# Performance work log

Measured on AMD Instinct MI355X. Metric: run time of the kernel, lower is better.

The kernel has to match this reference:

```python
import jax, jax.numpy as jnp
import numpy as np

B, T, C, H = 128, 256, 512, 512

def setup_inputs() -> dict:
    key = jax.random.key(0)
    k1, k2, k3, k4 = jax.random.split(key, 4)
    x = jax.random.normal(k1, (B, T, C), dtype=jnp.float32)
    # nn.Linear(n_embed, H_size, bias=False).weight has shape [H, C]; scaled init
    s = 1.0 / np.sqrt(C)
    Wq = jax.random.normal(k2, (H, C), dtype=jnp.float32) * s
    Wk = jax.random.normal(k3, (H, C), dtype=jnp.float32) * s
    Wv = jax.random.normal(k4, (H, C), dtype=jnp.float32) * s
    return {"x": x, "Wq": Wq, "Wk": Wk, "Wv": Wv}

def reference(x, Wq, Wk, Wv):
    # q,k,v: [B,T,H] = x @ W.T (torch Linear convention)
    q = jnp.einsum('btc,hc->bth', x, Wq)
    k = jnp.einsum('btc,hc->bth', x, Wk)
    v = jnp.einsum('btc,hc->bth', x, Wv)
    scale = k.shape[-1] ** -0.5
    score = jnp.einsum('bqh,bkh->bqk', q, k) * scale  # [B,T,T]
    # causal mask: position j attends to i only if i <= j
    i = jnp.arange(T)
    causal = i[None, :] <= i[:, None]  # [T,T] lower-triangular
    score = jnp.where(causal[None, :, :], score, -jnp.inf)
    attn = jax.nn.softmax(score, axis=-1)
    # dropout is identity in eval mode
    out = jnp.einsum('bqk,bkh->bqh', attn, v)  # [B,T,H]
    return out
```

## Files before the change

### kernel.cpp

```cpp
#include <hip/hip_runtime.h>

#define B_ 128
#define T_ 256
#define C_ 512
#define H_ 512
#define CSCALE 0.063763824f

typedef _Float16 f16x8 __attribute__((ext_vector_type(8)));
typedef _Float16 f16x4 __attribute__((ext_vector_type(4)));
typedef _Float16 f16x2 __attribute__((ext_vector_type(2)));
typedef float    f32x4 __attribute__((ext_vector_type(4)));
typedef float    f32x16 __attribute__((ext_vector_type(16)));
typedef unsigned int u32;
typedef u32 u32x4 __attribute__((ext_vector_type(4)));

__device__ __forceinline__ void gld16(const void* gsrc, void* ldst) {
  __builtin_amdgcn_global_load_lds(
      (__attribute__((address_space(1))) void*)gsrc,
      (__attribute__((address_space(3))) void*)ldst, 16, 0, 0);
}

__global__ __launch_bounds__(256) void cvt_kernel(
    const float4* __restrict__ x, const float4* __restrict__ wq,
    const float4* __restrict__ wk, const float4* __restrict__ wv,
    f16x4* __restrict__ dst) {
  const int NX = (B_ * T_ * C_) / 4;
  const int NW = (H_ * C_) / 4;
  const int total = NX + 3 * NW;
  int gid = blockIdx.x * 256 + threadIdx.x;
  int gsz = gridDim.x * 256;
  for (int i = gid; i < total; i += gsz) {
    float4 f;
    if (i < NX)            f = x[i];
    else if (i < NX + NW)  f = wq[i - NX];
    else if (i < NX + 2*NW) f = wk[i - NX - NW];
    else                   f = wv[i - NX - 2*NW];
    f16x4 u = {(_Float16)f.x, (_Float16)f.y, (_Float16)f.z, (_Float16)f.w};
    dst[i] = u;
  }
}

__global__ __launch_bounds__(256, 2) void proj_kernel(
    const _Float16* __restrict__ xh, const _Float16* __restrict__ wh,
    _Float16* __restrict__ qh, _Float16* __restrict__ kh,
    _Float16* __restrict__ vth) {
  __shared__ _Float16 L[3][2][4096];

  const int tid  = threadIdx.x;
  const int lane = tid & 63;
  const int wave = tid >> 6;
  const int lr = lane & 15, lk = lane >> 4;
  const int lane8 = lane * 8;
  const int m0 = blockIdx.x * 128;
  const int n0 = blockIdx.y * 128;
  const int z  = blockIdx.z;
  const _Float16* wz = wh + z * (H_ * C_);

  const int wm = (wave >> 1) * 64;
  const int wn = (wave & 1) * 64;
  const int ga = (wave >> 1) * 4;
  const int gb = (wave & 1) * 4;

  const _Float16* aS = xh + (size_t)(m0 + wave * 16 + lr) * C_ + lk * 8;
  const _Float16* bS = wz + (size_t)(n0 + wave * 16 + lr) * C_ + lk * 8;

  f32x4 acc[4][4];
#pragma unroll
  for (int i = 0; i < 4; ++i)
#pragma unroll
    for (int j = 0; j < 4; ++j) acc[i][j] = {0.f, 0.f, 0.f, 0.f};

#define STAGE(RB, K0) do {                                                    \
    gld16((const void*)(aS + (K0)),            (void*)&L[RB][0][wave * 512]); \
    gld16((const void*)(aS + 64 * C_ + (K0)),  (void*)&L[RB][0][(4 + wave) * 512]); \
    gld16((const void*)(bS + (K0)),            (void*)&L[RB][1][wave * 512]); \
    gld16((const void*)(bS + 64 * C_ + (K0)),  (void*)&L[RB][1][(4 + wave) * 512]); \
  } while (0)

  STAGE(0, 0);
  STAGE(1, 32);
  asm volatile("s_waitcnt vmcnt(4)" ::: "memory");
  __builtin_amdgcn_s_barrier();

#pragma unroll 1
  for (int t = 0; t < 16; ++t) {
    const int rb = t % 3;

    f16x8 af[4], bf[4];
#pragma unroll
    for (int mi = 0; mi < 4; ++mi)
      af[mi] = *(const f16x8*)&L[rb][0][(ga + mi) * 512 + lane8];
#pragma unroll
    for (int ni = 0; ni < 4; ++ni)
      bf[ni] = *(const f16x8*)&L[rb][1][(gb + ni) * 512 + lane8];

    if (t + 2 < 16) STAGE((t + 2) % 3, (t + 2) * 32);

    __builtin_amdgcn_s_setprio(1);
#pragma unroll
    for (int mi = 0; mi < 4; ++mi)
#pragma unroll
      for (int ni = 0; ni < 4; ++ni)
        acc[mi][ni] = __builtin_amdgcn_mfma_f32_16x16x32_f16(
            af[mi], bf[ni], acc[mi][ni], 0, 0, 0);
    __builtin_amdgcn_s_setprio(0);

    if (t + 2 < 16)      asm volatile("s_waitcnt vmcnt(4)" ::: "memory");
    else if (t == 14)    asm volatile("s_waitcnt vmcnt(0)" ::: "memory");
    __builtin_amdgcn_s_barrier();
  }
#undef STAGE

  if (z < 2) {
    _Float16* out = (z == 0) ? qh : kh;
#pragma unroll
    for (int mi = 0; mi < 4; ++mi) {
      int mg = m0 + wm + mi * 16 + lk * 4;
#pragma unroll
      for (int ni = 0; ni < 4; ++ni) {
        int n = n0 + wn + ni * 16 + lr;
#pragma unroll
        for (int r = 0; r < 4; ++r)
          out[(size_t)(mg + r) * H_ + n] = (_Float16)acc[mi][ni][r];
      }
    }
  } else {
#pragma unroll
    for (int mi = 0; mi < 4; ++mi) {
      int mbase = m0 + wm + mi * 16 + lk * 4;
      int bb = mbase >> 8, tt = mbase & 255;
#pragma unroll
      for (int ni = 0; ni < 4; ++ni) {
        int n = n0 + wn + ni * 16 + lr;
        f16x4 u = {(_Float16)acc[mi][ni][0], (_Float16)acc[mi][ni][1],
                   (_Float16)acc[mi][ni][2], (_Float16)acc[mi][ni][3]};
        *(f16x4*)&vth[(size_t)bb * (H_ * T_) + (size_t)n * T_ + tt] = u;
      }
    }
  }
}

__global__ __launch_bounds__(256, 2) void attn_kernel(
    const _Float16* __restrict__ qh, const _Float16* __restrict__ kh,
    const _Float16* __restrict__ vth, float* __restrict__ dout) {
  __shared__ f32x4 Ex[2][4][4][64];

  const int tid  = threadIdx.x;
  const int lane = tid & 63;
  const int wq   = tid >> 6;
  const int lq   = lane & 31;
  const int hi   = lane >> 5;
  const int flat = blockIdx.x;
  const int xcd  = flat & 7;
  const int rest = flat >> 3;
  const int qb   = 7 - (rest & 7);
  const int g    = rest >> 3;
  const int b    = xcd + (g << 3);
  const int q0   = qb * 32;
  const int nkv  = qb + 1;
  const int hbase = wq * 128;
  const int qg   = q0 + lq;

  f16x8 qf[8];
  const _Float16* qp = qh + ((size_t)b * T_ + qg) * H_ + hbase + hi * 8;
#pragma unroll
  for (int ks = 0; ks < 8; ++ks) qf[ks] = *(const f16x8*)&qp[ks * 16];

  f32x16 ot[4];
#pragma unroll
  for (int i = 0; i < 4; ++i) ot[i] = {};
  float m_ = -1e30f, l_ = 0.f;

  const _Float16* kp = kh  + ((size_t)b * T_ + lq) * H_ + hbase + hi * 8;
  const _Float16* vp = vth + ((size_t)b * H_ + hbase + lq) * T_ + hi * 8;

  f16x8 kf[8];
#pragma unroll
  for (int ks = 0; ks < 8; ++ks) kf[ks] = *(const f16x8*)&kp[ks * 16];
  {
    f32x16 s2 = {};
#pragma unroll
    for (int ks = 0; ks < 8; ++ks)
      s2 = __builtin_amdgcn_mfma_f32_32x32x16_f16(kf[ks], qf[ks], s2, 0, 0, 0);
#pragma unroll
    for (int c = 0; c < 4; ++c) {
      f32x4 w4 = {s2[c*4+0], s2[c*4+1], s2[c*4+2], s2[c*4+3]};
      Ex[0][wq][c][lane] = w4;
    }
  }

  for (int kvt = 0; kvt < nkv; ++kvt) {
    const int kv0 = kvt * 32;
    const int buf = kvt & 1;
    const bool more = (kvt + 1 < nkv);
    __syncthreads();

    f32x16 st;
#pragma unroll
    for (int c = 0; c < 4; ++c) {
      f32x4 r0 = Ex[buf][0][c][lane];
      f32x4 r1 = Ex[buf][1][c][lane];
      f32x4 r2 = Ex[buf][2][c][lane];
      f32x4 r3 = Ex[buf][3][c][lane];
      f32x4 r = (r0 + r1) + (r2 + r3);
      st[c*4+0] = r[0]; st[c*4+1] = r[1]; st[c*4+2] = r[2]; st[c*4+3] = r[3];
    }

    if (more) {
#pragma unroll
      for (int ks = 0; ks < 8; ++ks)
        kf[ks] = *(const f16x8*)&kp[(size_t)(kv0 + 32) * H_ + ks * 16];
    }

    float rm = -1e30f;
    const int kvb = kv0 + 4 * hi;
#pragma unroll
    for (int r = 0; r < 16; ++r) {
      int kvg = kvb + (r & 3) + 8 * (r >> 2);
      float v = (kvg > qg) ? -1e30f : st[r];
      st[r] = v;
      rm = fmaxf(rm, v);
    }
    rm = fmaxf(rm, __shfl_xor(rm, 32, 64));

    if (__any((int)(rm > m_ + 64.f))) {
      float mn = fmaxf(m_, rm);
      float al = __builtin_amdgcn_exp2f((m_ - mn) * CSCALE);
      m_ = mn; l_ *= al;
#pragma unroll
      for (int i = 0; i < 4; ++i)
#pragma unroll
        for (int e = 0; e < 16; ++e) ot[i][e] *= al;
    }
    float rs = 0.f;
#pragma unroll
    for (int r = 0; r < 16; ++r) {
      st[r] = __builtin_amdgcn_exp2f((st[r] - m_) * CSCALE);
      rs += st[r];
    }
    rs += __shfl_xor(rs, 32, 64);
    l_ += rs;

    f16x8 pb0, pb1;
    {
      f16x2 h0 = {(_Float16)st[0], (_Float16)st[1]};
      f16x2 h1 = {(_Float16)st[2], (_Float16)st[3]};
      f16x2 h2 = {(_Float16)st[4], (_Float16)st[5]};
      f16x2 h3 = {(_Float16)st[6], (_Float16)st[7]};
      u32 w0 = __builtin_bit_cast(u32, h0), w1 = __builtin_bit_cast(u32, h1);
      u32 w2 = __builtin_bit_cast(u32, h2), w3 = __builtin_bit_cast(u32, h3);
      u32 s0 = (u32)__shfl_xor((int)w0, 32, 64);
      u32 s1 = (u32)__shfl_xor((int)w1, 32, 64);
      u32 s2 = (u32)__shfl_xor((int)w2, 32, 64);
      u32 s3 = (u32)__shfl_xor((int)w3, 32, 64);
      u32x4 t0 = { hi ? s2 : w0, hi ? s3 : w1, hi ? w2 : s0, hi ? w3 : s1 };
      pb0 = __builtin_bit_cast(f16x8, t0);
    }
    {
      f16x2 h0 = {(_Float16)st[8],  (_Float16)st[9]};
      f16x2 h1 = {(_Float16)st[10], (_Float16)st[11]};
      f16x2 h2 = {(_Float16)st[12], (_Float16)st[13]};
      f16x2 h3 = {(_Float16)st[14], (_Float16)st[15]};
      u32 w0 = __builtin_bit_cast(u32, h0), w1 = __builtin_bit_cast(u32, h1);
      u32 w2 = __builtin_bit_cast(u32, h2), w3 = __builtin_bit_cast(u32, h3);
      u32 s0 = (u32)__shfl_xor((int)w0, 32, 64);
      u32 s1 = (u32)__shfl_xor((int)w1, 32, 64);
      u32 s2 = (u32)__shfl_xor((int)w2, 32, 64);
      u32 s3 = (u32)__shfl_xor((int)w3, 32, 64);
      u32x4 t1 = { hi ? s2 : w0, hi ? s3 : w1, hi ? w2 : s0, hi ? w3 : s1 };
      pb1 = __builtin_bit_cast(f16x8, t1);
    }

    __builtin_amdgcn_s_setprio(1);
#pragma unroll
    for (int ht = 0; ht < 4; ++ht) {
      f16x8 va0 = *(const f16x8*)&vp[(size_t)(ht * 32) * T_ + kv0];
      f16x8 va1 = *(const f16x8*)&vp[(size_t)(ht * 32) * T_ + kv0 + 16];
      ot[ht] = __builtin_amdgcn_mfma_f32_32x32x16_f16(va0, pb0, ot[ht], 0, 0, 0);
      ot[ht] = __builtin_amdgcn_mfma_f32_32x32x16_f16(va1, pb1, ot[ht], 0, 0, 0);
    }
    __builtin_amdgcn_s_setprio(0);

    if (more) {
      f32x16 s2v = {};
      __builtin_amdgcn_s_setprio(1);
#pragma unroll
      for (int ks = 0; ks < 8; ++ks)
        s2v = __builtin_amdgcn_mfma_f32_32x32x16_f16(kf[ks], qf[ks], s2v, 0, 0, 0);
      __builtin_amdgcn_s_setprio(0);
#pragma unroll
      for (int c = 0; c < 4; ++c) {
        f32x4 w4 = {s2v[c*4+0], s2v[c*4+1], s2v[c*4+2], s2v[c*4+3]};
        Ex[buf ^ 1][wq][c][lane] = w4;
      }
    }
  }

  float li = 1.0f / l_;
  float* op = dout + ((size_t)b * T_ + qg) * H_ + hbase + 4 * hi;
#pragma unroll
  for (int ht = 0; ht < 4; ++ht)
#pragma unroll
    for (int rq = 0; rq < 4; ++rq) {
      f32x4 v4 = {ot[ht][rq*4+0] * li, ot[ht][rq*4+1] * li,
                  ot[ht][rq*4+2] * li, ot[ht][rq*4+3] * li};
      *(f32x4*)&op[ht * 32 + rq * 8] = v4;
    }
}

extern "C" void kernel_launch(void* const* d_in, const int* in_sizes, int n_in,
                              void* d_out, int out_size, void* d_ws, size_t ws_size,
                              hipStream_t stream) {
  const size_t NXE = (size_t)B_ * T_ * C_;
  const size_t NWE = (size_t)3 * H_ * C_;
  const size_t NQE = (size_t)B_ * T_ * H_;
  const size_t need = (NXE + NWE + 3 * NQE) * sizeof(_Float16);
  if (ws_size < need) return;

  const float* x  = (const float*)d_in[0];
  const float* wq = (const float*)d_in[1];
  const float* wk = (const float*)d_in[2];
  const float* wv = (const float*)d_in[3];

  _Float16* xh  = (_Float16*)d_ws;
  _Float16* wh  = xh + NXE;
  _Float16* qh  = wh + NWE;
  _Float16* kh  = qh + NQE;
  _Float16* vth = kh + NQE;

  cvt_kernel<<<2048, 256, 0, stream>>>((const float4*)x, (const float4*)wq,
                                       (const float4*)wk, (const float4*)wv,
                                       (f16x4*)xh);
  proj_kernel<<<dim3(256, 4, 3), dim3(256), 0, stream>>>(xh, wh, qh, kh, vth);
  attn_kernel<<<1024, 256, 0, stream>>>(qh, kh, vth, (float*)d_out);
}
```

Before: 202.0 us.

## Simplify projection GEMM to single-buffer LDS loop and split conversion kernels

The projection kernel drops its triple-buffered global_load_lds pipeline with manual waitcnt and setprio in favour of a simple single-buffered loop bracketed by two __syncthreads per K step. The fp32-to-fp16 conversion is split into separate kernels for x and for the weights. The attention kernel now loads K fragments inline instead of prefetching them into registers, and its launch bound is raised to 3 blocks per SM to cut register use and raise occupancy. The cost is losing load/compute overlap in the GEMM and adding an extra kernel launch.

```diff
diff --git a/kernel.cpp b/kernel.cpp
--- a/kernel.cpp
+++ b/kernel.cpp
@@ -20,37 +20,40 @@
       (__attribute__((address_space(3))) void*)ldst, 16, 0, 0);
 }
 
-__global__ __launch_bounds__(256) void cvt_kernel(
-    const float4* __restrict__ x, const float4* __restrict__ wq,
-    const float4* __restrict__ wk, const float4* __restrict__ wv,
-    f16x4* __restrict__ dst) {
+__global__ __launch_bounds__(256) void cvtx_kernel(
+    const float4* __restrict__ x, f16x4* __restrict__ dst) {
   const int NX = (B_ * T_ * C_) / 4;
-  const int NW = (H_ * C_) / 4;
-  const int total = NX + 3 * NW;
   int gid = blockIdx.x * 256 + threadIdx.x;
   int gsz = gridDim.x * 256;
-  for (int i = gid; i < total; i += gsz) {
-    float4 f;
-    if (i < NX)            f = x[i];
-    else if (i < NX + NW)  f = wq[i - NX];
-    else if (i < NX + 2*NW) f = wk[i - NX - NW];
-    else                   f = wv[i - NX - 2*NW];
+  for (int i = gid; i < NX; i += gsz) {
+    float4 f = x[i];
     f16x4 u = {(_Float16)f.x, (_Float16)f.y, (_Float16)f.z, (_Float16)f.w};
     dst[i] = u;
   }
 }
 
-__global__ __launch_bounds__(256, 2) void proj_kernel(
+__global__ __launch_bounds__(256) void cvtw_kernel(
+    const float4* __restrict__ wq, const float4* __restrict__ wk,
+    const float4* __restrict__ wv, f16x4* __restrict__ dst) {
+  const int NW = (H_ * C_) / 4;
+  int i = blockIdx.x * 256 + threadIdx.x;
+  if (i >= 3 * NW) return;
+  float4 f = (i < NW) ? wq[i] : (i < 2 * NW ? wk[i - NW] : wv[i - 2 * NW]);
+  f16x4 u = {(_Float16)f.x, (_Float16)f.y, (_Float16)f.z, (_Float16)f.w};
+  dst[i] = u;
+}
+
+__global__ __launch_bounds__(256) void proj_kernel(
     const _Float16* __restrict__ xh, const _Float16* __restrict__ wh,
     _Float16* __restrict__ qh, _Float16* __restrict__ kh,
     _Float16* __restrict__ vth) {
-  __shared__ _Float16 L[3][2][4096];
+  __shared__ _Float16 As[128 * 32];
+  __shared__ _Float16 Bs[128 * 32];
 
   const int tid  = threadIdx.x;
   const int lane = tid & 63;
   const int wave = tid >> 6;
   const int lr = lane & 15, lk = lane >> 4;
-  const int lane8 = lane * 8;
   const int m0 = blockIdx.x * 128;
   const int n0 = blockIdx.y * 128;
   const int z  = blockIdx.z;
@@ -58,11 +61,6 @@
 
   const int wm = (wave >> 1) * 64;
   const int wn = (wave & 1) * 64;
-  const int ga = (wave >> 1) * 4;
-  const int gb = (wave & 1) * 4;
-
-  const _Float16* aS = xh + (size_t)(m0 + wave * 16 + lr) * C_ + lk * 8;
-  const _Float16* bS = wz + (size_t)(n0 + wave * 16 + lr) * C_ + lk * 8;
 
   f32x4 acc[4][4];
 #pragma unroll
@@ -70,58 +68,44 @@
 #pragma unroll
     for (int j = 0; j < 4; ++j) acc[i][j] = {0.f, 0.f, 0.f, 0.f};
 
-#define STAGE(RB, K0) do {                                                    \
-    gld16((const void*)(aS + (K0)),            (void*)&L[RB][0][wave * 512]); \
-    gld16((const void*)(aS + 64 * C_ + (K0)),  (void*)&L[RB][0][(4 + wave) * 512]); \
-    gld16((const void*)(bS + (K0)),            (void*)&L[RB][1][wave * 512]); \
-    gld16((const void*)(bS + 64 * C_ + (K0)),  (void*)&L[RB][1][(4 + wave) * 512]); \
-  } while (0)
-
-  STAGE(0, 0);
-  STAGE(1, 32);
-  asm volatile("s_waitcnt vmcnt(4)" ::: "memory");
-  __builtin_amdgcn_s_barrier();
-
-#pragma unroll 1
-  for (int t = 0; t < 16; ++t) {
-    const int rb = t % 3;
-
-    f16x8 af[4], bf[4];
+  const int srow = tid >> 2, scol = (tid & 3) * 8;
+  const _Float16* aSrc = xh + (size_t)(m0 + srow) * C_ + scol;
+  const _Float16* bSrc = wz + (size_t)(n0 + srow) * C_ + scol;
+
+  for (int k0 = 0; k0 < C_; k0 += 32) {
+    __syncthreads();
+#pragma unroll
+    for (int i = 0; i < 2; ++i) {
+      gld16((const void*)(aSrc + i * 64 * C_ + k0), (void*)&As[i * 2048 + wave * 512]);
+      gld16((const void*)(bSrc + i * 64 * C_ + k0), (void*)&Bs[i * 2048 + wave * 512]);
+    }
+    __syncthreads();
+
+    f16x8 a[4], b[4];
 #pragma unroll
     for (int mi = 0; mi < 4; ++mi)
-      af[mi] = *(const f16x8*)&L[rb][0][(ga + mi) * 512 + lane8];
+      a[mi] = *(const f16x8*)&As[(wm + mi * 16 + lr) * 32 + lk * 8];
 #pragma unroll
     for (int ni = 0; ni < 4; ++ni)
-      bf[ni] = *(const f16x8*)&L[rb][1][(gb + ni) * 512 + lane8];
-
-    if (t + 2 < 16) STAGE((t + 2) % 3, (t + 2) * 32);
-
-    __builtin_amdgcn_s_setprio(1);
+      b[ni] = *(const f16x8*)&Bs[(wn + ni * 16 + lr) * 32 + lk * 8];
 #pragma unroll
     for (int mi = 0; mi < 4; ++mi)
 #pragma unroll
       for (int ni = 0; ni < 4; ++ni)
-        acc[mi][ni] = __builtin_amdgcn_mfma_f32_16x16x32_f16(
-            af[mi], bf[ni], acc[mi][ni], 0, 0, 0);
-    __builtin_amdgcn_s_setprio(0);
-
-    if (t + 2 < 16)      asm volatile("s_waitcnt vmcnt(4)" ::: "memory");
-    else if (t == 14)    asm volatile("s_waitcnt vmcnt(0)" ::: "memory");
-    __builtin_amdgcn_s_barrier();
-  }
-#undef STAGE
+        acc[mi][ni] = __builtin_amdgcn_mfma_f32_16x16x32_f16(a[mi], b[ni], acc[mi][ni], 0, 0, 0);
+  }
 
   if (z < 2) {
     _Float16* out = (z == 0) ? qh : kh;
 #pragma unroll
     for (int mi = 0; mi < 4; ++mi) {
-      int mg = m0 + wm + mi * 16 + lk * 4;
+      int mbase = m0 + wm + mi * 16 + lk * 4;
 #pragma unroll
       for (int ni = 0; ni < 4; ++ni) {
         int n = n0 + wn + ni * 16 + lr;
 #pragma unroll
         for (int r = 0; r < 4; ++r)
-          out[(size_t)(mg + r) * H_ + n] = (_Float16)acc[mi][ni][r];
+          out[(size_t)(mbase + r) * H_ + n] = (_Float16)acc[mi][ni][r];
       }
     }
   } else {
@@ -140,7 +124,7 @@
   }
 }
 
-__global__ __launch_bounds__(256, 2) void attn_kernel(
+__global__ __launch_bounds__(256, 3) void attn_kernel(
     const _Float16* __restrict__ qh, const _Float16* __restrict__ kh,
     const _Float16* __restrict__ vth, float* __restrict__ dout) {
   __shared__ f32x4 Ex[2][4][4][64];
@@ -174,14 +158,13 @@
   const _Float16* kp = kh  + ((size_t)b * T_ + lq) * H_ + hbase + hi * 8;
   const _Float16* vp = vth + ((size_t)b * H_ + hbase + lq) * T_ + hi * 8;
 
-  f16x8 kf[8];
-#pragma unroll
-  for (int ks = 0; ks < 8; ++ks) kf[ks] = *(const f16x8*)&kp[ks * 16];
   {
     f32x16 s2 = {};
 #pragma unroll
-    for (int ks = 0; ks < 8; ++ks)
-      s2 = __builtin_amdgcn_mfma_f32_32x32x16_f16(kf[ks], qf[ks], s2, 0, 0, 0);
+    for (int ks = 0; ks < 8; ++ks) {
+      f16x8 kfv = *(const f16x8*)&kp[ks * 16];
+      s2 = __builtin_amdgcn_mfma_f32_32x32x16_f16(kfv, qf[ks], s2, 0, 0, 0);
+    }
 #pragma unroll
     for (int c = 0; c < 4; ++c) {
       f32x4 w4 = {s2[c*4+0], s2[c*4+1], s2[c*4+2], s2[c*4+3]};
@@ -204,12 +187,6 @@
       f32x4 r3 = Ex[buf][3][c][lane];
       f32x4 r = (r0 + r1) + (r2 + r3);
       st[c*4+0] = r[0]; st[c*4+1] = r[1]; st[c*4+2] = r[2]; st[c*4+3] = r[3];
-    }
-
-    if (more) {
-#pragma unroll
-      for (int ks = 0; ks < 8; ++ks)
-        kf[ks] = *(const f16x8*)&kp[(size_t)(kv0 + 32) * H_ + ks * 16];
     }
 
     float rm = -1e30f;
@@ -285,8 +262,10 @@
       f32x16 s2v = {};
       __builtin_amdgcn_s_setprio(1);
 #pragma unroll
-      for (int ks = 0; ks < 8; ++ks)
-        s2v = __builtin_amdgcn_mfma_f32_32x32x16_f16(kf[ks], qf[ks], s2v, 0, 0, 0);
+      for (int ks = 0; ks < 8; ++ks) {
+        f16x8 kfv = *(const f16x8*)&kp[(size_t)(kv0 + 32) * H_ + ks * 16];
+        s2v = __builtin_amdgcn_mfma_f32_32x32x16_f16(kfv, qf[ks], s2v, 0, 0, 0);
+      }
       __builtin_amdgcn_s_setprio(0);
 #pragma unroll
       for (int c = 0; c < 4; ++c) {
@@ -323,14 +302,14 @@
   const float* wv = (const float*)d_in[3];
 
   _Float16* xh  = (_Float16*)d_ws;
-  _Float16* wh  = xh + NXE;
-  _Float16* qh  = wh + NWE;
+  _Float16* whh = xh + NXE;
+  _Float16* qh  = whh + NWE;
   _Float16* kh  = qh + NQE;
   _Float16* vth = kh + NQE;
 
-  cvt_kernel<<<2048, 256, 0, stream>>>((const float4*)x, (const float4*)wq,
-                                       (const float4*)wk, (const float4*)wv,
-                                       (f16x4*)xh);
-  proj_kernel<<<dim3(256, 4, 3), dim3(256), 0, stream>>>(xh, wh, qh, kh, vth);
+  cvtx_kernel<<<2048, 256, 0, stream>>>((const float4*)x, (f16x4*)xh);
+  cvtw_kernel<<<768, 256, 0, stream>>>((const float4*)wq, (const float4*)wk,
+                                       (const float4*)wv, (f16x4*)whh);
+  proj_kernel<<<dim3(256, 4, 3), dim3(256), 0, stream>>>(xh, whh, qh, kh, vth);
   attn_kernel<<<1024, 256, 0, stream>>>(qh, kh, vth, (float*)d_out);
 }
```

Result: faster. 172.4 us (-14.7%).
